# Kernel tuning notes

Hardware: AMD Instinct MI355X
Metric: run time of the kernel (lower is better)

## Reference

```python
import jax, jax.numpy as jnp
import numpy as np

EMBED_DIM = 512
NUM_HEADS = 8
HEAD_DIM = EMBED_DIM // NUM_HEADS
K_NEIGH = 3
SEQ_N = 16384
BATCH = 4


def setup_inputs() -> dict:
    key = jax.random.key(0)
    ks = jax.random.split(key, 12)
    x = jax.random.normal(ks[0], (BATCH, SEQ_N, EMBED_DIM), dtype=jnp.float32)
    neighbor_table = jax.random.randint(ks[1], (K_NEIGH, SEQ_N), 0, SEQ_N, dtype=jnp.int64)
    s = 0.02
    Wq = jax.random.normal(ks[2], (EMBED_DIM, EMBED_DIM), jnp.float32) * s
    bq = jnp.zeros((EMBED_DIM,), jnp.float32)
    Wk = jax.random.normal(ks[3], (EMBED_DIM, EMBED_DIM), jnp.float32) * s
    bk = jnp.zeros((EMBED_DIM,), jnp.float32)
    Wv = jax.random.normal(ks[4], (EMBED_DIM, EMBED_DIM), jnp.float32) * s
    bv = jnp.zeros((EMBED_DIM,), jnp.float32)
    Wo = jax.random.normal(ks[5], (EMBED_DIM, EMBED_DIM), jnp.float32) * s
    bo = jnp.zeros((EMBED_DIM,), jnp.float32)
    return {"x": x, "neighbor_table": neighbor_table,
            "Wq": Wq, "bq": bq, "Wk": Wk, "bk": bk,
            "Wv": Wv, "bv": bv, "Wo": Wo, "bo": bo}


def reference(x, neighbor_table, Wq, bq, Wk, bk, Wv, bv, Wo, bo):
    B, N, C = x.shape
    H, d = NUM_HEADS, HEAD_DIM
    scale = d ** (-0.5)
    # buffers derived from neighbor_table (matches module __init__)
    valid = (neighbor_table != -1)                      # (K, N)
    idx = jnp.clip(neighbor_table, 0)                   # (K, N)

    # projections; nn.Linear: y = x @ W.T + b
    def proj(W, b):
        return (jnp.einsum('bnc,oc->bno', x, W) + b).reshape(B, N, H, d).transpose(0, 2, 1, 3)  # (B,H,N,d)

    q = proj(Wq, bq)
    k = proj(Wk, bk)
    v = proj(Wv, bv)

    # gather neighbors: (B, H, K, N, d)
    k_nb = k[:, :, idx, :]
    v_nb = v[:, :, idx, :]

    # scores over head_dim: (B, H, K, N)
    scores = jnp.einsum('bhnd,bhknd->bhkn', q, k_nb) * scale
    scores = jnp.where(valid[None, None], scores, -jnp.inf)
    attn = jax.nn.softmax(scores, axis=2)               # softmax over K neighbors
    # dropout is identity (eval / p used only at train)

    out = jnp.einsum('bhkn,bhknd->bhnd', attn, v_nb)    # (B,H,N,d)
    out = out.transpose(0, 2, 1, 3).reshape(B, N, C)
    out = jnp.einsum('bnc,oc->bno', out, Wo) + bo
    return out
```

## Files before the change

### kernel.cpp

```cpp
#include <hip/hip_runtime.h>
#include <stdint.h>

#define SEQN 16384
#define NBATCH 4

typedef __attribute__((ext_vector_type(8))) __bf16 bf16x8;
typedef __attribute__((ext_vector_type(4))) float f32x4;
typedef __attribute__((ext_vector_type(4))) unsigned int u32x4;

__device__ __forceinline__ unsigned int f2bf(float f) {
  unsigned int x = __builtin_bit_cast(unsigned int, f);
  x = x + 0x7fffu + ((x >> 16) & 1u);
  return x >> 16;
}
__device__ __forceinline__ float bf2f(unsigned int lo) {
  return __builtin_bit_cast(float, lo << 16);
}

__device__ __forceinline__ void gload_lds16(const unsigned short* g, unsigned char* l) {
  __builtin_amdgcn_global_load_lds(
      (const __attribute__((address_space(1))) unsigned int*)g,
      (__attribute__((address_space(3))) unsigned int*)l, 16, 0, 0);
}

template<bool OUT_BF16>
__global__ __launch_bounds__(256, 4)
void gemm_bt(const unsigned short* __restrict__ A,
             const unsigned short* __restrict__ Bt,
             const float* __restrict__ bias,
             void* __restrict__ Cout,
             int Ncols, int K)
{
  __shared__ __align__(16) unsigned char lds[32768];
  unsigned char* lA = lds;
  unsigned char* lB = lds + 16384;
  const int tid = threadIdx.x;
  const int lane = tid & 63;
  const int wid = tid >> 6;
  const int wr = (wid >> 1) * 64;
  const int wc = (wid & 1) * 64;
  const int nbx = Ncols >> 7;
  const int bid = (int)blockIdx.x;
  const int cpx = (int)gridDim.x >> 3;
  const int swz = (bid & 7) * cpx + (bid >> 3);
  const int bx = swz % nbx;
  const int by = swz / nbx;
  const long row0 = (long)by << 7;
  const int col0 = bx << 7;

  f32x4 acc[4][4];
#pragma unroll
  for (int i = 0; i < 4; ++i)
#pragma unroll
    for (int j = 0; j < 4; ++j) acc[i][j] = (f32x4)0.0f;

  for (int kt = 0; kt < K; kt += 64) {
#pragma unroll
    for (int i = 0; i < 4; ++i) {
      const int f = i * 256 + tid;
      const int r = f >> 3;
      const int cd = (f & 7) ^ (r & 7);
      gload_lds16(A + (row0 + r) * (long)K + kt + cd * 8, lA + f * 16);
      gload_lds16(Bt + (long)(col0 + r) * K + kt + cd * 8, lB + f * 16);
    }
    __syncthreads();
#pragma unroll
    for (int kk = 0; kk < 2; ++kk) {
      bf16x8 af[4], bfv[4];
#pragma unroll
      for (int fm = 0; fm < 4; ++fm) {
        const int row = wr + fm * 16 + (lane & 15);
        const int ch = (kk * 4 + (lane >> 4)) ^ (row & 7);
        af[fm] = __builtin_bit_cast(bf16x8, *(const u32x4*)(lA + row * 128 + ch * 16));
      }
#pragma unroll
      for (int fn = 0; fn < 4; ++fn) {
        const int row = wc + fn * 16 + (lane & 15);
        const int ch = (kk * 4 + (lane >> 4)) ^ (row & 7);
        bfv[fn] = __builtin_bit_cast(bf16x8, *(const u32x4*)(lB + row * 128 + ch * 16));
      }
#pragma unroll
      for (int fm = 0; fm < 4; ++fm)
#pragma unroll
        for (int fn = 0; fn < 4; ++fn)
          acc[fm][fn] = __builtin_amdgcn_mfma_f32_16x16x32_bf16(af[fm], bfv[fn], acc[fm][fn], 0, 0, 0);
    }
    __syncthreads();
  }

  if constexpr (OUT_BF16) {
#pragma unroll
    for (int fn = 0; fn < 4; ++fn) {
      const int n_loc = wc + fn * 16 + (lane & 15);
      const float bn = bias[col0 + n_loc];
#pragma unroll
      for (int fm = 0; fm < 4; ++fm) {
        const int rb = wr + fm * 16 + ((lane >> 4) << 2);
#pragma unroll
        for (int j = 0; j < 4; ++j) {
          const int row = rb + j;
          *(unsigned short*)(lds + row * 256 + ((n_loc * 2 + row * 32) & 255)) =
              (unsigned short)f2bf(acc[fm][fn][j] + bn);
        }
      }
    }
    __syncthreads();
#pragma unroll
    for (int i = 0; i < 8; ++i) {
      const int chunk = i * 256 + tid;
      const int row = chunk >> 4;
      const int co = (chunk & 15) * 16;
      const u32x4 v = *(const u32x4*)(lds + row * 256 + ((co + row * 32) & 255));
      *(u32x4*)((unsigned short*)Cout + (row0 + row) * (long)Ncols + col0 + (co >> 1)) = v;
    }
  } else {
#pragma unroll
    for (int fn = 0; fn < 4; ++fn) {
      const int n = col0 + wc + fn * 16 + (lane & 15);
      const float bn = bias[n];
#pragma unroll
      for (int fm = 0; fm < 4; ++fm) {
        const long mbase = row0 + wr + fm * 16 + ((lane >> 4) << 2);
#pragma unroll
        for (int j = 0; j < 4; ++j)
          ((float*)Cout)[(mbase + j) * (long)Ncols + n] = acc[fm][fn][j] + bn;
      }
    }
  }
}

__global__ __launch_bounds__(256)
void nbr_attn(const unsigned short* __restrict__ qkv,
              const int* __restrict__ nbr,
              unsigned short* __restrict__ aout)
{
  const int w = (int)((blockIdx.x * 256 + threadIdx.x) >> 6);
  const int lane = threadIdx.x & 63;
  const int r0 = w * 2;
  const int n0 = r0 & (SEQN - 1);
  const int b  = r0 >> 14;

  const unsigned short* qr = qkv + (size_t)r0 * 1536;
  const u32x4 q0raw = *(const u32x4*)(qr + lane * 8);
  const u32x4 q1raw = *(const u32x4*)(qr + 1536 + lane * 8);

  int t[6];
  t[0] = nbr[n0];            t[3] = nbr[n0 + 1];
  t[1] = nbr[SEQN + n0];     t[4] = nbr[SEQN + n0 + 1];
  t[2] = nbr[2 * SEQN + n0]; t[5] = nbr[2 * SEQN + n0 + 1];

  const unsigned short* base = qkv + (size_t)b * SEQN * 1536 + 512 + lane * 8;
  u32x4 kr[6], vr[6];
#pragma unroll
  for (int k = 0; k < 6; ++k) {
    const unsigned short* p = base + (size_t)(t[k] > 0 ? t[k] : 0) * 1536;
    kr[k] = *(const u32x4*)p;
    vr[k] = *(const u32x4*)(p + 512);
  }

  float qv0[8], qv1[8];
#pragma unroll
  for (int i = 0; i < 4; ++i) {
    qv0[2 * i] = bf2f(q0raw[i] & 0xffffu);
    qv0[2 * i + 1] = bf2f(q0raw[i] >> 16);
    qv1[2 * i] = bf2f(q1raw[i] & 0xffffu);
    qv1[2 * i + 1] = bf2f(q1raw[i] >> 16);
  }

  float s[6];
#pragma unroll
  for (int k = 0; k < 6; ++k) {
    const float* q = (k < 3) ? qv0 : qv1;
    float d = 0.f;
#pragma unroll
    for (int i = 0; i < 4; ++i)
      d += q[2 * i] * bf2f(kr[k][i] & 0xffffu) + q[2 * i + 1] * bf2f(kr[k][i] >> 16);
    d += __shfl_xor(d, 1);
    d += __shfl_xor(d, 2);
    d += __shfl_xor(d, 4);
    s[k] = d * 0.125f;
  }

#pragma unroll
  for (int rrow = 0; rrow < 2; ++rrow) {
    const int o = rrow * 3;
    float m = -3.0e38f;
#pragma unroll
    for (int k = 0; k < 3; ++k)
      if (t[o + k] != -1) m = fmaxf(m, s[o + k]);
    float e[3], sum = 0.f;
#pragma unroll
    for (int k = 0; k < 3; ++k) {
      e[k] = (t[o + k] != -1) ? __expf(s[o + k] - m) : 0.f;
      sum += e[k];
    }
    const float inv = sum > 0.f ? 1.f / sum : 0.f;
    float acc[8] = {0.f, 0.f, 0.f, 0.f, 0.f, 0.f, 0.f, 0.f};
#pragma unroll
    for (int k = 0; k < 3; ++k) {
      const float wgt = e[k] * inv;
#pragma unroll
      for (int i = 0; i < 4; ++i) {
        acc[2 * i] += wgt * bf2f(vr[o + k][i] & 0xffffu);
        acc[2 * i + 1] += wgt * bf2f(vr[o + k][i] >> 16);
      }
    }
    u32x4 ov;
#pragma unroll
    for (int i = 0; i < 4; ++i)
      ov[i] = f2bf(acc[2 * i]) | (f2bf(acc[2 * i + 1]) << 16);
    *(u32x4*)(aout + (size_t)(r0 + rrow) * 512 + lane * 8) = ov;
  }
}

__global__ __launch_bounds__(256)
void cvt_prep(const float* __restrict__ x, unsigned short* __restrict__ xb,
              const float* __restrict__ Wq, const float* __restrict__ Wk,
              const float* __restrict__ Wv, const float* __restrict__ Wo,
              const float* __restrict__ bq, const float* __restrict__ bk,
              const float* __restrict__ bv,
              unsigned short* __restrict__ wf, unsigned short* __restrict__ wo,
              float* __restrict__ biasf)
{
  const int i = blockIdx.x * 256 + threadIdx.x;
  if (i < 262144) {
    wf[i] = (unsigned short)f2bf(Wq[i]);
    wf[262144 + i] = (unsigned short)f2bf(Wk[i]);
    wf[524288 + i] = (unsigned short)f2bf(Wv[i]);
    wo[i] = (unsigned short)f2bf(Wo[i]);
  }
  if (i < 512) {
    biasf[i] = bq[i];
    biasf[512 + i] = bk[i];
    biasf[1024 + i] = bv[i];
  }
#pragma unroll
  for (int t = i; t < 4194304; t += 1048576) {
    const float4* p = (const float4*)(x + (size_t)t * 8);
    const float4 a = p[0], c = p[1];
    u32x4 o;
    o[0] = f2bf(a.x) | (f2bf(a.y) << 16);
    o[1] = f2bf(a.z) | (f2bf(a.w) << 16);
    o[2] = f2bf(c.x) | (f2bf(c.y) << 16);
    o[3] = f2bf(c.z) | (f2bf(c.w) << 16);
    *(u32x4*)(xb + (size_t)t * 8) = o;
  }
}

extern "C" void kernel_launch(void* const* d_in, const int* in_sizes, int n_in,
                              void* d_out, int out_size, void* d_ws, size_t ws_size,
                              hipStream_t stream) {
  const float* x  = (const float*)d_in[0];
  const int* nbr  = (const int*)d_in[1];
  const float* Wq = (const float*)d_in[2];
  const float* bq = (const float*)d_in[3];
  const float* Wk = (const float*)d_in[4];
  const float* bk = (const float*)d_in[5];
  const float* Wv = (const float*)d_in[6];
  const float* bv = (const float*)d_in[7];
  const float* Wo = (const float*)d_in[8];
  const float* bo = (const float*)d_in[9];
  float* out = (float*)d_out;
  unsigned char* ws = (unsigned char*)d_ws;

  unsigned short* xb  = (unsigned short*)(ws);
  unsigned short* qkv = (unsigned short*)(ws + 67108864UL);
  unsigned short* wf  = (unsigned short*)(ws + 268435456UL);
  unsigned short* wo  = (unsigned short*)(ws + 270008320UL);
  float* biasf        = (float*)(ws + 270532608UL);

  cvt_prep<<<4096, 256, 0, stream>>>(x, xb, Wq, Wk, Wv, Wo, bq, bk, bv, wf, wo, biasf);
  gemm_bt<true><<<dim3(512 * 12), 256, 0, stream>>>(xb, wf, biasf, qkv, 1536, 512);
  nbr_attn<<<8192, 256, 0, stream>>>(qkv, nbr, xb);
  gemm_bt<false><<<dim3(512 * 4), 256, 0, stream>>>(xb, wo, bo, out, 512, 512);
}
```

Measured before the change: 282.0 us.

## Fuse fp32-to-bf16 conversion of x into the QKV GEMM tile loads

Removes the standalone conversion pass over x and has the QKV GEMM load fp32 tiles directly into LDS, converting to bf16 when building MFMA fragments. This avoids writing and rereading a bf16 copy of x. In exchange, each GEMM tile load moves twice the bytes, the conversion is repeated across every output column tile, and LDS per block grows to 48KB, which may reduce occupancy.

```diff
diff --git a/kernel.cpp b/kernel.cpp
--- a/kernel.cpp
+++ b/kernel.cpp
@@ -17,23 +17,22 @@
   return __builtin_bit_cast(float, lo << 16);
 }
 
-__device__ __forceinline__ void gload_lds16(const unsigned short* g, unsigned char* l) {
+__device__ __forceinline__ void gload_lds16(const void* g, unsigned char* l) {
   __builtin_amdgcn_global_load_lds(
       (const __attribute__((address_space(1))) unsigned int*)g,
       (__attribute__((address_space(3))) unsigned int*)l, 16, 0, 0);
 }
 
-template<bool OUT_BF16>
 __global__ __launch_bounds__(256, 4)
-void gemm_bt(const unsigned short* __restrict__ A,
-             const unsigned short* __restrict__ Bt,
-             const float* __restrict__ bias,
-             void* __restrict__ Cout,
-             int Ncols, int K)
+void gemm_qkv(const float* __restrict__ A,
+              const unsigned short* __restrict__ Bt,
+              const float* __restrict__ bias,
+              unsigned short* __restrict__ Cout,
+              int Ncols, int K)
 {
-  __shared__ __align__(16) unsigned char lds[32768];
-  unsigned char* lA = lds;
-  unsigned char* lB = lds + 16384;
+  __shared__ __align__(16) unsigned char lds[49152];
+  unsigned char* lAf = lds;
+  unsigned char* lB  = lds + 32768;
   const int tid = threadIdx.x;
   const int lane = tid & 63;
   const int wid = tid >> 6;
@@ -60,6 +59,111 @@
       const int f = i * 256 + tid;
       const int r = f >> 3;
       const int cd = (f & 7) ^ (r & 7);
+      gload_lds16(Bt + (long)(col0 + r) * K + kt + cd * 8, lB + f * 16);
+    }
+#pragma unroll
+    for (int i = 0; i < 8; ++i) {
+      const int G = i * 256 + tid;
+      const int r = G >> 4;
+      const int c = G & 15;
+      const int p = (c & 7) ^ (r & 7);
+      const int esrc = p * 8 + ((c >> 3) << 2);
+      gload_lds16(A + (row0 + r) * (long)K + kt + esrc, lAf + G * 16);
+    }
+    __syncthreads();
+#pragma unroll
+    for (int kk = 0; kk < 2; ++kk) {
+      bf16x8 af[4], bfv[4];
+#pragma unroll
+      for (int fm = 0; fm < 4; ++fm) {
+        const int row = wr + fm * 16 + (lane & 15);
+        const int P = kk * 4 + (lane >> 4);
+        const int off = row * 256 + (((P ^ (row & 7))) << 4);
+        const float4 lo = *(const float4*)(lAf + off);
+        const float4 hi = *(const float4*)(lAf + off + 128);
+        bf16x8 a;
+        a[0] = (__bf16)lo.x; a[1] = (__bf16)lo.y;
+        a[2] = (__bf16)lo.z; a[3] = (__bf16)lo.w;
+        a[4] = (__bf16)hi.x; a[5] = (__bf16)hi.y;
+        a[6] = (__bf16)hi.z; a[7] = (__bf16)hi.w;
+        af[fm] = a;
+      }
+#pragma unroll
+      for (int fn = 0; fn < 4; ++fn) {
+        const int row = wc + fn * 16 + (lane & 15);
+        const int ch = (kk * 4 + (lane >> 4)) ^ (row & 7);
+        bfv[fn] = __builtin_bit_cast(bf16x8, *(const u32x4*)(lB + row * 128 + ch * 16));
+      }
+#pragma unroll
+      for (int fm = 0; fm < 4; ++fm)
+#pragma unroll
+        for (int fn = 0; fn < 4; ++fn)
+          acc[fm][fn] = __builtin_amdgcn_mfma_f32_16x16x32_bf16(af[fm], bfv[fn], acc[fm][fn], 0, 0, 0);
+    }
+    __syncthreads();
+  }
+
+#pragma unroll
+  for (int fn = 0; fn < 4; ++fn) {
+    const int n_loc = wc + fn * 16 + (lane & 15);
+    const float bn = bias[col0 + n_loc];
+#pragma unroll
+    for (int fm = 0; fm < 4; ++fm) {
+      const int rb = wr + fm * 16 + ((lane >> 4) << 2);
+#pragma unroll
+      for (int j = 0; j < 4; ++j) {
+        const int row = rb + j;
+        *(unsigned short*)(lds + row * 256 + ((n_loc * 2 + row * 32) & 255)) =
+            (unsigned short)f2bf(acc[fm][fn][j] + bn);
+      }
+    }
+  }
+  __syncthreads();
+#pragma unroll
+  for (int i = 0; i < 8; ++i) {
+    const int chunk = i * 256 + tid;
+    const int row = chunk >> 4;
+    const int co = (chunk & 15) * 16;
+    const u32x4 v = *(const u32x4*)(lds + row * 256 + ((co + row * 32) & 255));
+    *(u32x4*)(Cout + (row0 + row) * (long)Ncols + col0 + (co >> 1)) = v;
+  }
+}
+
+__global__ __launch_bounds__(256, 4)
+void gemm_bt_f32out(const unsigned short* __restrict__ A,
+                    const unsigned short* __restrict__ Bt,
+                    const float* __restrict__ bias,
+                    float* __restrict__ Cout,
+                    int Ncols, int K)
+{
+  __shared__ __align__(16) unsigned char lA[128 * 64 * 2];
+  __shared__ __align__(16) unsigned char lB[128 * 64 * 2];
+  const int tid = threadIdx.x;
+  const int lane = tid & 63;
+  const int wid = tid >> 6;
+  const int wr = (wid >> 1) * 64;
+  const int wc = (wid & 1) * 64;
+  const int nbx = Ncols >> 7;
+  const int bid = (int)blockIdx.x;
+  const int cpx = (int)gridDim.x >> 3;
+  const int swz = (bid & 7) * cpx + (bid >> 3);
+  const int bx = swz % nbx;
+  const int by = swz / nbx;
+  const long row0 = (long)by << 7;
+  const int col0 = bx << 7;
+
+  f32x4 acc[4][4];
+#pragma unroll
+  for (int i = 0; i < 4; ++i)
+#pragma unroll
+    for (int j = 0; j < 4; ++j) acc[i][j] = (f32x4)0.0f;
+
+  for (int kt = 0; kt < K; kt += 64) {
+#pragma unroll
+    for (int i = 0; i < 4; ++i) {
+      const int f = i * 256 + tid;
+      const int r = f >> 3;
+      const int cd = (f & 7) ^ (r & 7);
       gload_lds16(A + (row0 + r) * (long)K + kt + cd * 8, lA + f * 16);
       gload_lds16(Bt + (long)(col0 + r) * K + kt + cd * 8, lB + f * 16);
     }
@@ -88,43 +192,16 @@
     __syncthreads();
   }
 
-  if constexpr (OUT_BF16) {
-#pragma unroll
-    for (int fn = 0; fn < 4; ++fn) {
-      const int n_loc = wc + fn * 16 + (lane & 15);
-      const float bn = bias[col0 + n_loc];
-#pragma unroll
-      for (int fm = 0; fm < 4; ++fm) {
-        const int rb = wr + fm * 16 + ((lane >> 4) << 2);
-#pragma unroll
-        for (int j = 0; j < 4; ++j) {
-          const int row = rb + j;
-          *(unsigned short*)(lds + row * 256 + ((n_loc * 2 + row * 32) & 255)) =
-              (unsigned short)f2bf(acc[fm][fn][j] + bn);
-        }
-      }
-    }
-    __syncthreads();
-#pragma unroll
-    for (int i = 0; i < 8; ++i) {
-      const int chunk = i * 256 + tid;
-      const int row = chunk >> 4;
-      const int co = (chunk & 15) * 16;
-      const u32x4 v = *(const u32x4*)(lds + row * 256 + ((co + row * 32) & 255));
-      *(u32x4*)((unsigned short*)Cout + (row0 + row) * (long)Ncols + col0 + (co >> 1)) = v;
-    }
-  } else {
-#pragma unroll
-    for (int fn = 0; fn < 4; ++fn) {
-      const int n = col0 + wc + fn * 16 + (lane & 15);
-      const float bn = bias[n];
-#pragma unroll
-      for (int fm = 0; fm < 4; ++fm) {
-        const long mbase = row0 + wr + fm * 16 + ((lane >> 4) << 2);
-#pragma unroll
-        for (int j = 0; j < 4; ++j)
-          ((float*)Cout)[(mbase + j) * (long)Ncols + n] = acc[fm][fn][j] + bn;
-      }
+#pragma unroll
+  for (int fn = 0; fn < 4; ++fn) {
+    const int n = col0 + wc + fn * 16 + (lane & 15);
+    const float bn = bias[n];
+#pragma unroll
+    for (int fm = 0; fm < 4; ++fm) {
+      const long mbase = row0 + wr + fm * 16 + ((lane >> 4) << 2);
+#pragma unroll
+      for (int j = 0; j < 4; ++j)
+        Cout[(mbase + j) * (long)Ncols + n] = acc[fm][fn][j] + bn;
     }
   }
 }
@@ -214,13 +291,12 @@
 }
 
 __global__ __launch_bounds__(256)
-void cvt_prep(const float* __restrict__ x, unsigned short* __restrict__ xb,
-              const float* __restrict__ Wq, const float* __restrict__ Wk,
-              const float* __restrict__ Wv, const float* __restrict__ Wo,
-              const float* __restrict__ bq, const float* __restrict__ bk,
-              const float* __restrict__ bv,
-              unsigned short* __restrict__ wf, unsigned short* __restrict__ wo,
-              float* __restrict__ biasf)
+void prep_w(const float* __restrict__ Wq, const float* __restrict__ Wk,
+            const float* __restrict__ Wv, const float* __restrict__ Wo,
+            const float* __restrict__ bq, const float* __restrict__ bk,
+            const float* __restrict__ bv,
+            unsigned short* __restrict__ wf, unsigned short* __restrict__ wo,
+            float* __restrict__ biasf)
 {
   const int i = blockIdx.x * 256 + threadIdx.x;
   if (i < 262144) {
@@ -233,17 +309,6 @@
     biasf[i] = bq[i];
     biasf[512 + i] = bk[i];
     biasf[1024 + i] = bv[i];
-  }
-#pragma unroll
-  for (int t = i; t < 4194304; t += 1048576) {
-    const float4* p = (const float4*)(x + (size_t)t * 8);
-    const float4 a = p[0], c = p[1];
-    u32x4 o;
-    o[0] = f2bf(a.x) | (f2bf(a.y) << 16);
-    o[1] = f2bf(a.z) | (f2bf(a.w) << 16);
-    o[2] = f2bf(c.x) | (f2bf(c.y) << 16);
-    o[3] = f2bf(c.z) | (f2bf(c.w) << 16);
-    *(u32x4*)(xb + (size_t)t * 8) = o;
   }
 }
 
@@ -263,14 +328,14 @@
   float* out = (float*)d_out;
   unsigned char* ws = (unsigned char*)d_ws;
 
-  unsigned short* xb  = (unsigned short*)(ws);
+  unsigned short* ao  = (unsigned short*)(ws);
   unsigned short* qkv = (unsigned short*)(ws + 67108864UL);
   unsigned short* wf  = (unsigned short*)(ws + 268435456UL);
   unsigned short* wo  = (unsigned short*)(ws + 270008320UL);
   float* biasf        = (float*)(ws + 270532608UL);
 
-  cvt_prep<<<4096, 256, 0, stream>>>(x, xb, Wq, Wk, Wv, Wo, bq, bk, bv, wf, wo, biasf);
-  gemm_bt<true><<<dim3(512 * 12), 256, 0, stream>>>(xb, wf, biasf, qkv, 1536, 512);
-  nbr_attn<<<8192, 256, 0, stream>>>(qkv, nbr, xb);
-  gemm_bt<false><<<dim3(512 * 4), 256, 0, stream>>>(xb, wo, bo, out, 512, 512);
-}
+  prep_w<<<1024, 256, 0, stream>>>(Wq, Wk, Wv, Wo, bq, bk, bv, wf, wo, biasf);
+  gemm_qkv<<<dim3(512 * 12), 256, 0, stream>>>(x, wf, biasf, qkv, 1536, 512);
+  nbr_attn<<<8192, 256, 0, stream>>>(qkv, nbr, ao);
+  gemm_bt_f32out<<<dim3(512 * 4), 256, 0, stream>>>(ao, wo, bo, out, 512, 512);
+}
```

Result: slower. 362.7 us (+28.6%).
